# Kernel optimization log

Hardware: AMD Instinct MI355X
Metric: run time of the kernel (lower is better)

The kernel has to match this reference:

```python
import jax, jax.numpy as jnp
import numpy as np

B, C, L = 32, 256, 4096

def _bn(x, g, b, m, v, eps=1e-5):
    # x: [B, C, L]; eval-mode batchnorm with running stats
    inv = jax.lax.rsqrt(v + eps)
    return (x - m[None, :, None]) * (inv * g)[None, :, None] + b[None, :, None]

def _ln(x, g, b, eps=1e-6):
    # layernorm over last dim
    mu = jnp.mean(x, axis=-1, keepdims=True)
    var = jnp.mean(jnp.square(x - mu), axis=-1, keepdims=True)
    return (x - mu) * jax.lax.rsqrt(var + eps) * g + b

def _conv1d(x, w, stride=1):
    # x: [B, Cin, L], w: [Cout, Cin, K]
    return jax.lax.conv_general_dilated(
        x, w, window_strides=(stride,), padding=[(1, 1)],
        dimension_numbers=('NCW', 'OIW', 'NCW'))

def _dct2_matrix(n, dtype):
    # scipy.fftpack.dct type-II, norm=None: y[k] = 2*sum_n x[n]*cos(pi*k*(2n+1)/(2N))
    k = jnp.arange(n, dtype=dtype)[:, None]
    m = jnp.arange(n, dtype=dtype)[None, :]
    return 2.0 * jnp.cos(jnp.pi * k * (2.0 * m + 1.0) / (2.0 * n))


def setup_inputs() -> dict:
    key = jax.random.key(0)
    ks = jax.random.split(key, 12)
    s_conv = 1.0 / np.sqrt(C * 3)
    s_fc1 = 1.0 / np.sqrt(C)
    s_fc2 = 1.0 / np.sqrt(2 * C)
    return {
        'x': jax.random.normal(ks[0], (B, C, L), jnp.float32),
        'conv1_w': jax.random.normal(ks[1], (C, C, 3), jnp.float32) * s_conv,
        'bn1_g': jnp.ones((C,), jnp.float32),
        'bn1_b': jnp.zeros((C,), jnp.float32),
        'bn1_m': jax.random.normal(ks[2], (C,), jnp.float32) * 0.1,
        'bn1_v': jax.random.uniform(ks[3], (C,), jnp.float32, 0.5, 1.5),
        'conv2_w': jax.random.normal(ks[4], (C, C, 3), jnp.float32) * s_conv,
        'bn2_g': jnp.ones((C,), jnp.float32),
        'bn2_b': jnp.zeros((C,), jnp.float32),
        'bn2_m': jax.random.normal(ks[5], (C,), jnp.float32) * 0.1,
        'bn2_v': jax.random.uniform(ks[6], (C,), jnp.float32, 0.5, 1.5),
        'fc1_w': jax.random.normal(ks[7], (2 * C, C), jnp.float32) * s_fc1,
        'fc2_w': jax.random.normal(ks[8], (C, 2 * C), jnp.float32) * s_fc2,
        'ln_g': jnp.ones((C,), jnp.float32),
        'ln_b': jnp.zeros((C,), jnp.float32),
    }


def reference(x, conv1_w, bn1_g, bn1_b, bn1_m, bn1_v,
              conv2_w, bn2_g, bn2_b, bn2_m, bn2_v,
              fc1_w, fc2_w, ln_g, ln_b):
    out = _bn(_conv1d(x, conv1_w), bn1_g, bn1_b, bn1_m, bn1_v)
    out = jax.nn.relu(out)
    out = _bn(_conv1d(out, conv2_w), bn2_g, bn2_b, bn2_m, bn2_v)

    # ---- FECAM (faithful to source: DCT-II along the channel axis) ----
    xp = jnp.transpose(out, (0, 2, 1))  # [B, L, C]
    Dm = _dct2_matrix(xp.shape[-1], xp.dtype)  # [C, C]
    freq = jnp.einsum('bln,kn->blk', xp, Dm)   # DCT over channel dim
    sd = _ln(freq, ln_g, ln_b)
    h = jax.nn.relu(jnp.einsum('blc,hc->blh', sd, fc1_w))      # C -> 2C
    fw = jax.nn.sigmoid(jnp.einsum('blh,ch->blc', h, fc2_w))   # 2C -> C
    fw = _ln(fw, ln_g, ln_b)  # same LayerNorm module applied again
    out = jnp.transpose(xp * fw, (0, 2, 1))  # [B, C, L]

    # inplanes == planes, stride == 1 -> identity downsample
    return jax.nn.relu(out + x)
```

## Files before the change

kernel.cpp:

```cpp
#include <hip/hip_runtime.h>
#include <math.h>

#define BB 32
#define CC 256
#define LL 4096

typedef __attribute__((ext_vector_type(8))) short bf16x8;
typedef __attribute__((ext_vector_type(4))) float f32x4;

__device__ __forceinline__ unsigned short f2bf(float f) {
  unsigned u = __float_as_uint(f);
  u = (u + 0x7FFFu + ((u >> 16) & 1u)) >> 16;
  return (unsigned short)u;
}
__device__ __forceinline__ float bf2f(unsigned short v) {
  return __uint_as_float(((unsigned)v) << 16);
}

__global__ void init_bias(const float* __restrict__ g1, const float* __restrict__ b1,
                          const float* __restrict__ m1, const float* __restrict__ v1,
                          const float* __restrict__ g2, const float* __restrict__ b2,
                          const float* __restrict__ m2, const float* __restrict__ v2,
                          float* __restrict__ b1f, float* __restrict__ b2f) {
  int c = threadIdx.x;
  b1f[c] = b1[c] - m1[c] * g1[c] * rsqrtf(v1[c] + 1e-5f);
  b2f[c] = b2[c] - m2[c] * g2[c] * rsqrtf(v2[c] + 1e-5f);
}

__global__ void init_wsw(const float* __restrict__ w1, const float* __restrict__ g1,
                         const float* __restrict__ v1,
                         const float* __restrict__ w2, const float* __restrict__ g2,
                         const float* __restrict__ v2,
                         unsigned short* __restrict__ W1sw, unsigned short* __restrict__ W2sw) {
  int id = blockIdx.x * 256 + threadIdx.x;
  int cv = id / 196608;
  int i = id - cv * 196608;
  int kc3t = i >> 13;
  int kc = kc3t / 3, t = kc3t - 3 * kc;
  int rem = i & 8191;
  int nt = rem >> 9, L = (rem >> 3) & 63, j = i & 7;
  int co = nt * 16 + (L & 15);
  int ci = kc * 32 + ((L >> 4) << 3) + j;
  if (cv == 0) {
    float s = g1[co] * rsqrtf(v1[co] + 1e-5f);
    W1sw[i] = f2bf(w1[(co * 256 + ci) * 3 + t] * s);
  } else {
    float s = g2[co] * rsqrtf(v2[co] + 1e-5f);
    W2sw[i] = f2bf(w2[(co * 256 + ci) * 3 + t] * s);
  }
}

__global__ void init_bsw(const float* __restrict__ fc1, const float* __restrict__ fc2,
                         unsigned short* __restrict__ Bd, unsigned short* __restrict__ B1,
                         unsigned short* __restrict__ B2) {
  int id = blockIdx.x * 256 + threadIdx.x;
  if (id < 65536) {
    int i = id;
    int kc = i >> 13, nt = (i >> 9) & 15, L = (i >> 3) & 63, j = i & 7;
    int n = nt * 16 + (L & 15), k = kc * 32 + (L >> 4) * 8 + j;
    double v = 2.0 * cos(3.14159265358979323846 * (double)n * (2.0 * k + 1.0) / 512.0);
    Bd[i] = f2bf((float)v);
  } else if (id < 65536 + 131072) {
    int i = id - 65536;
    int kc = i >> 14, nt = (i >> 9) & 31, L = (i >> 3) & 63, j = i & 7;
    int n = nt * 16 + (L & 15), k = kc * 32 + (L >> 4) * 8 + j;
    B1[i] = f2bf(fc1[n * 256 + k]);
  } else {
    int i = id - 65536 - 131072;
    int kc = i >> 13, nt = (i >> 9) & 15, L = (i >> 3) & 63, j = i & 7;
    int n = nt * 16 + (L & 15), k = kc * 32 + (L >> 4) * 8 + j;
    B2[i] = f2bf(fc2[n * 512 + k]);
  }
}

__global__ __launch_bounds__(256) void transpose_x(const float* __restrict__ x,
                                                   unsigned short* __restrict__ xT) {
  __shared__ unsigned short ts[64][68];
  const int tid = threadIdx.x;
  const int b = blockIdx.z, ci0 = blockIdx.y << 6, l0 = blockIdx.x << 6;
#pragma unroll
  for (int p = 0; p < 4; ++p) {
    int cc = (p << 4) + (tid >> 4);
    int ll = (tid & 15) << 2;
    float4 v = *(const float4*)&x[((((size_t)b << 8) + ci0 + cc) << 12) + l0 + ll];
    ts[ll + 0][cc] = f2bf(v.x);
    ts[ll + 1][cc] = f2bf(v.y);
    ts[ll + 2][cc] = f2bf(v.z);
    ts[ll + 3][cc] = f2bf(v.w);
  }
  __syncthreads();
#pragma unroll
  for (int p = 0; p < 4; ++p) {
    int idx = tid + (p << 8);
    int row = idx >> 4, ch = idx & 15;
    uint2 v = *(const uint2*)&ts[row][ch << 2];
    *(uint2*)&xT[((((size_t)b << 12) + l0 + row) << 8) + ci0 + (ch << 2)] = v;
  }
}

template <bool RELU, bool FRAGOUT>
__global__ __launch_bounds__(256, 4) void conv_mfma(
    const unsigned short* __restrict__ inT, const unsigned short* __restrict__ Wsw,
    const float* __restrict__ bias, unsigned short* __restrict__ outT) {
  __shared__ char smem[34848];
  unsigned short* xs = (unsigned short*)smem;
  unsigned short* swz = (unsigned short*)smem;

  const int tid = threadIdx.x;
  const int w = tid >> 6, lane = tid & 63;
  const int g = lane >> 4, c = lane & 15;
  const int l0 = blockIdx.x << 6;
  const int b = blockIdx.y;
  const size_t rowbase = ((size_t)b << 12) + l0;

  for (int idx = tid; idx < 66 * 32; idx += 256) {
    int r = idx >> 5, ch = idx & 31;
    int gl = l0 - 1 + r;
    uint4 v = {0, 0, 0, 0};
    if (gl >= 0 && gl < LL)
      v = *(const uint4*)&inT[((((size_t)b << 12) + gl) << 8) + (ch << 3)];
    *(uint4*)&xs[r * 264 + (ch << 3)] = v;
  }
  __syncthreads();

  f32x4 acc[4][4];
#pragma unroll
  for (int i = 0; i < 4; ++i)
#pragma unroll
    for (int j = 0; j < 4; ++j) acc[i][j] = (f32x4){0.f, 0.f, 0.f, 0.f};

  for (int kc = 0; kc < 8; ++kc)
#pragma unroll
    for (int t = 0; t < 3; ++t) {
      const unsigned short* src = Wsw + ((kc * 3 + t) << 13);
      bf16x8 af[4];
#pragma unroll
      for (int mt = 0; mt < 4; ++mt)
        af[mt] = *(const bf16x8*)&xs[(mt * 16 + c + t) * 264 + (kc << 5) + (g << 3)];
#pragma unroll
      for (int nt = 0; nt < 4; ++nt) {
        bf16x8 bfv = *(const bf16x8*)&src[(((w << 2) + nt) << 9) + (lane << 3)];
#pragma unroll
        for (int mt = 0; mt < 4; ++mt)
          acc[mt][nt] = __builtin_amdgcn_mfma_f32_16x16x32_bf16(af[mt], bfv, acc[mt][nt], 0, 0, 0);
      }
    }
  __syncthreads();

  float pb[4];
#pragma unroll
  for (int nt = 0; nt < 4; ++nt) pb[nt] = bias[(w << 6) + nt * 16 + c];
#pragma unroll
  for (int mt = 0; mt < 4; ++mt)
#pragma unroll
    for (int r = 0; r < 4; ++r) {
      int row = mt * 16 + g * 4 + r;
#pragma unroll
      for (int nt = 0; nt < 4; ++nt) {
        float v = acc[mt][nt][r] + pb[nt];
        if (RELU) v = fmaxf(v, 0.f);
        swz[row * 264 + (w << 6) + nt * 16 + c] = f2bf(v);
      }
    }
  __syncthreads();
  if (!FRAGOUT) {
#pragma unroll
    for (int i = 0; i < 8; ++i) {
      int idx = tid + (i << 8);
      int row = idx >> 5, ch = idx & 31;
      *(uint4*)&outT[((rowbase + row) << 8) + (ch << 3)] = *(const uint4*)&swz[row * 264 + (ch << 3)];
    }
  } else {
    const int MT0 = (int)(rowbase >> 4);
#pragma unroll
    for (int i = 0; i < 8; ++i) {
      int f = tid + (i << 8);
      int mtl = f >> 9, kcl = (f >> 6) & 7, L = f & 63;
      int row = mtl * 16 + (L & 15), k0 = (kcl << 5) + ((L >> 4) << 3);
      uint4 v = *(const uint4*)&swz[row * 264 + k0];
      *(uint4*)&outT[(((size_t)(MT0 + mtl) * 8 + kcl) << 9) + L * 8] = v;
    }
  }
}

__global__ __launch_bounds__(256, 3) void gemm_fused(
    const unsigned short* __restrict__ xp, const unsigned short* __restrict__ Bd,
    const unsigned short* __restrict__ B1, const unsigned short* __restrict__ B2,
    const float* __restrict__ lng, const float* __restrict__ lnb,
    const float* __restrict__ xin, float* __restrict__ outp) {
  __shared__ char smem[43008];
  unsigned short* sdS = (unsigned short*)smem;
  unsigned short* hS = (unsigned short*)(smem + 32768);
  float* ps1 = (float*)(smem + 40960);
  float* ps2 = (float*)(smem + 40960 + 1024);
  unsigned short* swz = (unsigned short*)smem;

  const int tid = threadIdx.x;
  const int w = tid >> 6;
  const int lane = tid & 63;
  const int g = lane >> 4, c = lane & 15;
  const int MT0 = blockIdx.x << 2;

  float pg[4], pb[4];
#pragma unroll
  for (int nt = 0; nt < 4; ++nt) {
    int col = (w << 6) + nt * 16 + c;
    pg[nt] = lng[col]; pb[nt] = lnb[col];
  }

  {
    f32x4 a0[4][4];
#pragma unroll
    for (int i = 0; i < 4; ++i)
#pragma unroll
      for (int j = 0; j < 4; ++j) a0[i][j] = (f32x4){0.f, 0.f, 0.f, 0.f};

    for (int kc = 0; kc < 8; ++kc) {
      bf16x8 af[4];
#pragma unroll
      for (int mt = 0; mt < 4; ++mt)
        af[mt] = *(const bf16x8*)(xp + (((size_t)(MT0 + mt) << 3) + kc) * 512 + lane * 8);
#pragma unroll
      for (int nt = 0; nt < 4; ++nt) {
        bf16x8 bfv = *(const bf16x8*)(Bd + (((size_t)kc << 4) + (w << 2) + nt) * 512 + lane * 8);
#pragma unroll
        for (int mt = 0; mt < 4; ++mt)
          a0[mt][nt] = __builtin_amdgcn_mfma_f32_16x16x32_bf16(af[mt], bfv, a0[mt][nt], 0, 0, 0);
      }
    }

#pragma unroll
    for (int mt = 0; mt < 4; ++mt)
#pragma unroll
      for (int r = 0; r < 4; ++r) {
        float s1 = 0.f, s2 = 0.f;
#pragma unroll
        for (int nt = 0; nt < 4; ++nt) { float v = a0[mt][nt][r]; s1 += v; s2 += v * v; }
#pragma unroll
        for (int m = 1; m < 16; m <<= 1) { s1 += __shfl_xor(s1, m, 64); s2 += __shfl_xor(s2, m, 64); }
        if (c == 0) {
          ps1[(w << 6) + mt * 16 + g * 4 + r] = s1;
          ps2[(w << 6) + mt * 16 + g * 4 + r] = s2;
        }
      }
    __syncthreads();
#pragma unroll
    for (int mt = 0; mt < 4; ++mt)
#pragma unroll
      for (int r = 0; r < 4; ++r) {
        int row = mt * 16 + g * 4 + r;
        float s1 = ps1[row] + ps1[64 + row] + ps1[128 + row] + ps1[192 + row];
        float s2 = ps2[row] + ps2[64 + row] + ps2[128 + row] + ps2[192 + row];
        float mu = s1 * (1.f / 256.f);
        float var = s2 * (1.f / 256.f) - mu * mu;
        float inv = 1.f / sqrtf(var + 1e-6f);
#pragma unroll
        for (int nt = 0; nt < 4; ++nt) {
          int col = (w << 6) + nt * 16 + c;
          float v = (a0[mt][nt][r] - mu) * inv * pg[nt] + pb[nt];
          sdS[((mt << 3) + (col >> 5)) * 512 + (((((col >> 3) & 3) << 4) | (row & 15)) << 3) +
              (col & 7)] = f2bf(v);
        }
      }
    __syncthreads();
  }

  f32x4 acc[4][4];
#pragma unroll
  for (int i = 0; i < 4; ++i)
#pragma unroll
    for (int j = 0; j < 4; ++j) acc[i][j] = (f32x4){0.f, 0.f, 0.f, 0.f};

  for (int hc = 0; hc < 8; ++hc) {
    f32x4 a1[4];
#pragma unroll
    for (int mt = 0; mt < 4; ++mt) a1[mt] = (f32x4){0.f, 0.f, 0.f, 0.f};
    const unsigned short* b1p = B1 + (size_t)((hc << 2) + w) * 512 + lane * 8;
    for (int kc = 0; kc < 8; ++kc) {
      bf16x8 bfv = *(const bf16x8*)(b1p + (size_t)kc * 16384);
#pragma unroll
      for (int mt = 0; mt < 4; ++mt) {
        bf16x8 af = *(const bf16x8*)&sdS[((mt << 3) + kc) * 512 + lane * 8];
        a1[mt] = __builtin_amdgcn_mfma_f32_16x16x32_bf16(af, bfv, a1[mt], 0, 0, 0);
      }
    }
#pragma unroll
    for (int mt = 0; mt < 4; ++mt)
#pragma unroll
      for (int r = 0; r < 4; ++r) {
        int row = mt * 16 + g * 4 + r;
        float v = fmaxf(a1[mt][r], 0.f);
        hS[((mt << 1) + (w >> 1)) * 512 +
           ((((((w & 1) << 1) | (c >> 3)) << 4) | (row & 15)) << 3) + (c & 7)] = f2bf(v);
      }
    __syncthreads();
#pragma unroll
    for (int kcl = 0; kcl < 2; ++kcl) {
      bf16x8 af2[4];
#pragma unroll
      for (int mt = 0; mt < 4; ++mt)
        af2[mt] = *(const bf16x8*)&hS[((mt << 1) + kcl) * 512 + lane * 8];
#pragma unroll
      for (int nt = 0; nt < 4; ++nt) {
        bf16x8 bfv = *(const bf16x8*)(B2 + (size_t)((((hc << 1) + kcl) << 4) + (w << 2) + nt) * 512 +
                                      lane * 8);
#pragma unroll
        for (int mt = 0; mt < 4; ++mt)
          acc[mt][nt] = __builtin_amdgcn_mfma_f32_16x16x32_bf16(af2[mt], bfv, acc[mt][nt], 0, 0, 0);
      }
    }
    __syncthreads();
  }

#pragma unroll
  for (int mt = 0; mt < 4; ++mt)
#pragma unroll
    for (int nt = 0; nt < 4; ++nt)
#pragma unroll
      for (int r = 0; r < 4; ++r)
        acc[mt][nt][r] = 1.f / (1.f + expf(-acc[mt][nt][r]));
#pragma unroll
  for (int mt = 0; mt < 4; ++mt)
#pragma unroll
    for (int r = 0; r < 4; ++r) {
      float s1 = 0.f, s2 = 0.f;
#pragma unroll
      for (int nt = 0; nt < 4; ++nt) { float v = acc[mt][nt][r]; s1 += v; s2 += v * v; }
#pragma unroll
      for (int m = 1; m < 16; m <<= 1) { s1 += __shfl_xor(s1, m, 64); s2 += __shfl_xor(s2, m, 64); }
      if (c == 0) {
        ps1[(w << 6) + mt * 16 + g * 4 + r] = s1;
        ps2[(w << 6) + mt * 16 + g * 4 + r] = s2;
      }
    }
  __syncthreads();
  float mu_[4][4], inv_[4][4];
#pragma unroll
  for (int mt = 0; mt < 4; ++mt)
#pragma unroll
    for (int r = 0; r < 4; ++r) {
      int row = mt * 16 + g * 4 + r;
      float s1 = ps1[row] + ps1[64 + row] + ps1[128 + row] + ps1[192 + row];
      float s2 = ps2[row] + ps2[64 + row] + ps2[128 + row] + ps2[192 + row];
      float mu = s1 * (1.f / 256.f);
      float var = s2 * (1.f / 256.f) - mu * mu;
      mu_[mt][r] = mu;
      inv_[mt][r] = 1.f / sqrtf(var + 1e-6f);
    }
#pragma unroll
  for (int mt = 0; mt < 4; ++mt)
#pragma unroll
    for (int nt = 0; nt < 4; ++nt) {
      alignas(8) unsigned short tmp[4];
#pragma unroll
      for (int r = 0; r < 4; ++r)
        tmp[r] = f2bf((acc[mt][nt][r] - mu_[mt][r]) * inv_[mt][r] * pg[nt] + pb[nt]);
      int col = (w << 6) + nt * 16 + c;
      *(uint2*)&swz[col * 68 + mt * 16 + g * 4] = *(const uint2*)tmp;
    }
  __syncthreads();
  {
    const int row0 = MT0 << 4;
    const int b = row0 >> 12;
    const int l0 = row0 & 4095;
    const int li = tid & 63, cq = tid >> 6;
    for (int i = 0; i < 64; ++i) {
      int ccol = cq * 64 + i;
      float fwv = bf2f(swz[ccol * 68 + li]);
      size_t xoff = (((size_t)(MT0 + (li >> 4)) * 8 + (ccol >> 5)) << 9) +
                    (((((ccol >> 3) & 3) << 4) + (li & 15)) << 3) + (ccol & 7);
      float xpv = bf2f(xp[xoff]);
      size_t o = ((size_t)((b << 8) + ccol)) * LL + l0 + li;
      float ov = fmaf(xpv, fwv, xin[o]);
      outp[o] = fmaxf(ov, 0.f);
    }
  }
}

extern "C" void kernel_launch(void* const* d_in, const int* in_sizes, int n_in,
                              void* d_out, int out_size, void* d_ws, size_t ws_size,
                              hipStream_t stream) {
  const float* x    = (const float*)d_in[0];
  const float* w1   = (const float*)d_in[1];
  const float* g1   = (const float*)d_in[2];
  const float* b1   = (const float*)d_in[3];
  const float* m1   = (const float*)d_in[4];
  const float* v1   = (const float*)d_in[5];
  const float* w2   = (const float*)d_in[6];
  const float* g2   = (const float*)d_in[7];
  const float* b2   = (const float*)d_in[8];
  const float* m2   = (const float*)d_in[9];
  const float* v2   = (const float*)d_in[10];
  const float* fc1  = (const float*)d_in[11];
  const float* fc2  = (const float*)d_in[12];
  const float* lng  = (const float*)d_in[13];
  const float* lnb  = (const float*)d_in[14];
  float* out = (float*)d_out;

  float* ws = (float*)d_ws;
  float* b1f = ws;
  float* b2f = ws + 256;
  unsigned short* Bd   = (unsigned short*)(ws + 512);
  unsigned short* B1   = (unsigned short*)(ws + 33280);
  unsigned short* B2   = (unsigned short*)(ws + 98816);
  unsigned short* W1sw = (unsigned short*)(ws + 164352);
  unsigned short* W2sw = (unsigned short*)(ws + 262656);
  unsigned short* xT    = (unsigned short*)(ws + 360960);
  unsigned short* y1T  = (unsigned short*)(ws + 17138176);
  unsigned short* xp_sw = (unsigned short*)(ws + 50692608);

  init_bias<<<1, 256, 0, stream>>>(g1, b1, m1, v1, g2, b2, m2, v2, b1f, b2f);
  init_wsw<<<1536, 256, 0, stream>>>(w1, g1, v1, w2, g2, v2, W1sw, W2sw);
  init_bsw<<<1280, 256, 0, stream>>>(fc1, fc2, Bd, B1, B2);

  transpose_x<<<dim3(64, 4, 32), 256, 0, stream>>>(x, xT);

  conv_mfma<true, false><<<dim3(64, 32), 256, 0, stream>>>(xT, W1sw, b1f, y1T);
  conv_mfma<false, true><<<dim3(64, 32), 256, 0, stream>>>(y1T, W2sw, b2f, xp_sw);

  gemm_fused<<<2048, 256, 0, stream>>>(xp_sw, Bd, B1, B2, lng, lnb, x, out);
}
```

Before: 622.5 us.

## Stage conv weights via LDS direct loads, swizzle GEMM LDS, vectorize epilogue

The conv kernel now stages each weight slice into shared memory with global_load_lds and barriers, instead of having every wave read weights directly from global memory. Occupancy hints move to 3 blocks for conv and 4 for gemm_fused. gemm_fused also XOR-swizzles its shared-memory A-fragment layout to avoid bank conflicts, switches to fast rsq, rcp and exp intrinsics, and loads xp as 8-wide vectors in the final residual epilogue. The extra barriers per conv k-step and the lower conv occupancy may offset the weight-staging gain.

```diff
diff --git a/kernel.cpp b/kernel.cpp
--- a/kernel.cpp
+++ b/kernel.cpp
@@ -15,6 +15,13 @@
 }
 __device__ __forceinline__ float bf2f(unsigned short v) {
   return __uint_as_float(((unsigned)v) << 16);
+}
+__device__ __forceinline__ int swz16(int blk) { return blk ^ ((blk >> 3) & 7); }
+
+__device__ __forceinline__ void gload_lds16(const unsigned short* g, unsigned short* l) {
+  __builtin_amdgcn_global_load_lds(
+      (const __attribute__((address_space(1))) unsigned int*)g,
+      (__attribute__((address_space(3))) unsigned int*)l, 16, 0, 0);
 }
 
 __global__ void init_bias(const float* __restrict__ g1, const float* __restrict__ b1,
@@ -58,8 +65,9 @@
     int i = id;
     int kc = i >> 13, nt = (i >> 9) & 15, L = (i >> 3) & 63, j = i & 7;
     int n = nt * 16 + (L & 15), k = kc * 32 + (L >> 4) * 8 + j;
-    double v = 2.0 * cos(3.14159265358979323846 * (double)n * (2.0 * k + 1.0) / 512.0);
-    Bd[i] = f2bf((float)v);
+    int m = (n * (2 * k + 1)) & 1023;
+    float v = 2.0f * cosf(3.14159265358979323846f * (float)m * (1.0f / 512.0f));
+    Bd[i] = f2bf(v);
   } else if (id < 65536 + 131072) {
     int i = id - 65536;
     int kc = i >> 14, nt = (i >> 9) & 31, L = (i >> 3) & 63, j = i & 7;
@@ -99,11 +107,12 @@
 }
 
 template <bool RELU, bool FRAGOUT>
-__global__ __launch_bounds__(256, 4) void conv_mfma(
+__global__ __launch_bounds__(256, 3) void conv_mfma(
     const unsigned short* __restrict__ inT, const unsigned short* __restrict__ Wsw,
     const float* __restrict__ bias, unsigned short* __restrict__ outT) {
-  __shared__ char smem[34848];
+  __shared__ char smem[51232];
   unsigned short* xs = (unsigned short*)smem;
+  unsigned short* smemB = (unsigned short*)(smem + 34848);
   unsigned short* swz = (unsigned short*)smem;
 
   const int tid = threadIdx.x;
@@ -121,7 +130,6 @@
       v = *(const uint4*)&inT[((((size_t)b << 12) + gl) << 8) + (ch << 3)];
     *(uint4*)&xs[r * 264 + (ch << 3)] = v;
   }
-  __syncthreads();
 
   f32x4 acc[4][4];
 #pragma unroll
@@ -132,14 +140,24 @@
   for (int kc = 0; kc < 8; ++kc)
 #pragma unroll
     for (int t = 0; t < 3; ++t) {
+      __syncthreads();
       const unsigned short* src = Wsw + ((kc * 3 + t) << 13);
+      {
+        const unsigned short* gs = src + (w << 11) + (lane << 3);
+        unsigned short* ls = smemB + (w << 11);
+        gload_lds16(gs, ls);
+        gload_lds16(gs + 512, ls + 512);
+        gload_lds16(gs + 1024, ls + 1024);
+        gload_lds16(gs + 1536, ls + 1536);
+      }
+      __syncthreads();
       bf16x8 af[4];
 #pragma unroll
       for (int mt = 0; mt < 4; ++mt)
         af[mt] = *(const bf16x8*)&xs[(mt * 16 + c + t) * 264 + (kc << 5) + (g << 3)];
 #pragma unroll
       for (int nt = 0; nt < 4; ++nt) {
-        bf16x8 bfv = *(const bf16x8*)&src[(((w << 2) + nt) << 9) + (lane << 3)];
+        bf16x8 bfv = *(const bf16x8*)&smemB[((w << 2) + nt) * 512 + (lane << 3)];
 #pragma unroll
         for (int mt = 0; mt < 4; ++mt)
           acc[mt][nt] = __builtin_amdgcn_mfma_f32_16x16x32_bf16(af[mt], bfv, acc[mt][nt], 0, 0, 0);
@@ -183,16 +201,16 @@
   }
 }
 
-__global__ __launch_bounds__(256, 3) void gemm_fused(
+__global__ __launch_bounds__(256, 4) void gemm_fused(
     const unsigned short* __restrict__ xp, const unsigned short* __restrict__ Bd,
     const unsigned short* __restrict__ B1, const unsigned short* __restrict__ B2,
     const float* __restrict__ lng, const float* __restrict__ lnb,
     const float* __restrict__ xin, float* __restrict__ outp) {
-  __shared__ char smem[43008];
+  __shared__ char smem[40960];
   unsigned short* sdS = (unsigned short*)smem;
   unsigned short* hS = (unsigned short*)(smem + 32768);
-  float* ps1 = (float*)(smem + 40960);
-  float* ps2 = (float*)(smem + 40960 + 1024);
+  float* ps1 = (float*)(smem + 36864);
+  float* ps2 = (float*)(smem + 37888);
   unsigned short* swz = (unsigned short*)smem;
 
   const int tid = threadIdx.x;
@@ -200,6 +218,7 @@
   const int lane = tid & 63;
   const int g = lane >> 4, c = lane & 15;
   const int MT0 = blockIdx.x << 2;
+  const int lsw8 = swz16(lane) * 8;
 
   float pg[4], pb[4];
 #pragma unroll
@@ -248,18 +267,19 @@
     for (int mt = 0; mt < 4; ++mt)
 #pragma unroll
       for (int r = 0; r < 4; ++r) {
-        int row = mt * 16 + g * 4 + r;
-        float s1 = ps1[row] + ps1[64 + row] + ps1[128 + row] + ps1[192 + row];
-        float s2 = ps2[row] + ps2[64 + row] + ps2[128 + row] + ps2[192 + row];
+        int row15 = g * 4 + r;
+        int rr = mt * 16 + row15;
+        float s1 = ps1[rr] + ps1[64 + rr] + ps1[128 + rr] + ps1[192 + rr];
+        float s2 = ps2[rr] + ps2[64 + rr] + ps2[128 + rr] + ps2[192 + rr];
         float mu = s1 * (1.f / 256.f);
         float var = s2 * (1.f / 256.f) - mu * mu;
-        float inv = 1.f / sqrtf(var + 1e-6f);
+        float inv = __builtin_amdgcn_rsqf(var + 1e-6f);
 #pragma unroll
         for (int nt = 0; nt < 4; ++nt) {
           int col = (w << 6) + nt * 16 + c;
           float v = (a0[mt][nt][r] - mu) * inv * pg[nt] + pb[nt];
-          sdS[((mt << 3) + (col >> 5)) * 512 + (((((col >> 3) & 3) << 4) | (row & 15)) << 3) +
-              (col & 7)] = f2bf(v);
+          int blk = (((col >> 3) & 3) << 4) | row15;
+          sdS[((mt << 3) + (col >> 5)) * 512 + swz16(blk) * 8 + (col & 7)] = f2bf(v);
         }
       }
     __syncthreads();
@@ -280,7 +300,7 @@
       bf16x8 bfv = *(const bf16x8*)(b1p + (size_t)kc * 16384);
 #pragma unroll
       for (int mt = 0; mt < 4; ++mt) {
-        bf16x8 af = *(const bf16x8*)&sdS[((mt << 3) + kc) * 512 + lane * 8];
+        bf16x8 af = *(const bf16x8*)&sdS[((mt << 3) + kc) * 512 + lsw8];
         a1[mt] = __builtin_amdgcn_mfma_f32_16x16x32_bf16(af, bfv, a1[mt], 0, 0, 0);
       }
     }
@@ -288,10 +308,10 @@
     for (int mt = 0; mt < 4; ++mt)
 #pragma unroll
       for (int r = 0; r < 4; ++r) {
-        int row = mt * 16 + g * 4 + r;
+        int row15 = g * 4 + r;
         float v = fmaxf(a1[mt][r], 0.f);
-        hS[((mt << 1) + (w >> 1)) * 512 +
-           ((((((w & 1) << 1) | (c >> 3)) << 4) | (row & 15)) << 3) + (c & 7)] = f2bf(v);
+        int blk = (((((w & 1) << 1) | (c >> 3))) << 4) | row15;
+        hS[((mt << 1) + (w >> 1)) * 512 + swz16(blk) * 8 + (c & 7)] = f2bf(v);
       }
     __syncthreads();
 #pragma unroll
@@ -299,7 +319,7 @@
       bf16x8 af2[4];
 #pragma unroll
       for (int mt = 0; mt < 4; ++mt)
-        af2[mt] = *(const bf16x8*)&hS[((mt << 1) + kcl) * 512 + lane * 8];
+        af2[mt] = *(const bf16x8*)&hS[((mt << 1) + kcl) * 512 + lsw8];
 #pragma unroll
       for (int nt = 0; nt < 4; ++nt) {
         bf16x8 bfv = *(const bf16x8*)(B2 + (size_t)((((hc << 1) + kcl) << 4) + (w << 2) + nt) * 512 +
@@ -318,7 +338,7 @@
     for (int nt = 0; nt < 4; ++nt)
 #pragma unroll
       for (int r = 0; r < 4; ++r)
-        acc[mt][nt][r] = 1.f / (1.f + expf(-acc[mt][nt][r]));
+        acc[mt][nt][r] = __builtin_amdgcn_rcpf(1.f + __expf(-acc[mt][nt][r]));
 #pragma unroll
   for (int mt = 0; mt < 4; ++mt)
 #pragma unroll
@@ -339,13 +359,13 @@
   for (int mt = 0; mt < 4; ++mt)
 #pragma unroll
     for (int r = 0; r < 4; ++r) {
-      int row = mt * 16 + g * 4 + r;
-      float s1 = ps1[row] + ps1[64 + row] + ps1[128 + row] + ps1[192 + row];
-      float s2 = ps2[row] + ps2[64 + row] + ps2[128 + row] + ps2[192 + row];
+      int rr = mt * 16 + g * 4 + r;
+      float s1 = ps1[rr] + ps1[64 + rr] + ps1[128 + rr] + ps1[192 + rr];
+      float s2 = ps2[rr] + ps2[64 + rr] + ps2[128 + rr] + ps2[192 + rr];
       float mu = s1 * (1.f / 256.f);
       float var = s2 * (1.f / 256.f) - mu * mu;
       mu_[mt][r] = mu;
-      inv_[mt][r] = 1.f / sqrtf(var + 1e-6f);
+      inv_[mt][r] = __builtin_amdgcn_rsqf(var + 1e-6f);
     }
 #pragma unroll
   for (int mt = 0; mt < 4; ++mt)
@@ -364,15 +384,22 @@
     const int b = row0 >> 12;
     const int l0 = row0 & 4095;
     const int li = tid & 63, cq = tid >> 6;
-    for (int i = 0; i < 64; ++i) {
-      int ccol = cq * 64 + i;
-      float fwv = bf2f(swz[ccol * 68 + li]);
-      size_t xoff = (((size_t)(MT0 + (li >> 4)) * 8 + (ccol >> 5)) << 9) +
-                    (((((ccol >> 3) & 3) << 4) + (li & 15)) << 3) + (ccol & 7);
-      float xpv = bf2f(xp[xoff]);
-      size_t o = ((size_t)((b << 8) + ccol)) * LL + l0 + li;
-      float ov = fmaf(xpv, fwv, xin[o]);
-      outp[o] = fmaxf(ov, 0.f);
+    const size_t xbase = (size_t)(MT0 + (li >> 4)) * 4096 + (size_t)(li & 15) * 8;
+    const size_t obase = ((size_t)((b << 8) + (cq << 6))) * LL + l0 + li;
+#pragma unroll
+    for (int i8 = 0; i8 < 8; ++i8) {
+      bf16x8 xq = *(const bf16x8*)&xp[xbase + (size_t)((cq << 1) + (i8 >> 2)) * 512 +
+                                      (size_t)(i8 & 3) * 128];
+#pragma unroll
+      for (int j = 0; j < 8; ++j) {
+        int ic = (i8 << 3) + j;
+        int ccol = (cq << 6) + ic;
+        float fwv = bf2f(swz[ccol * 68 + li]);
+        float xpv = bf2f((unsigned short)xq[j]);
+        size_t o = obase + (size_t)ic * LL;
+        float ov = fmaf(xpv, fwv, xin[o]);
+        outp[o] = fmaxf(ov, 0.f);
+      }
     }
   }
 }
```

Result: no change. 614.4 us (-1.3%).
